# Optimization experiments

Hardware: AMD Instinct MI355X
Metric: run time of the kernel (lower is better)

The kernel has to match this reference:

```python
import jax, jax.numpy as jnp
import numpy as np

RADIUS = 1.3
RES = 256
N_INT = 128
STEP = 0.02


def grid_sample3d(grid, coords):
    # grid: [C, D, H, W]; coords: [N, 3] as (x, y, z) in [-1, 1]
    # trilinear, align_corners=True, border clamp (torch grid_sample semantics)
    D, H, W = grid.shape[1], grid.shape[2], grid.shape[3]

    def to_idx(c, size):
        return jnp.clip((c + 1.0) * 0.5 * (size - 1), 0.0, size - 1.0)

    x = to_idx(coords[:, 0], W)
    y = to_idx(coords[:, 1], H)
    z = to_idx(coords[:, 2], D)
    x0 = jnp.floor(x).astype(jnp.int32)
    y0 = jnp.floor(y).astype(jnp.int32)
    z0 = jnp.floor(z).astype(jnp.int32)
    x1 = jnp.minimum(x0 + 1, W - 1)
    y1 = jnp.minimum(y0 + 1, H - 1)
    z1 = jnp.minimum(z0 + 1, D - 1)
    wx = x - x0.astype(x.dtype)
    wy = y - y0.astype(y.dtype)
    wz = z - z0.astype(z.dtype)

    def g(zi, yi, xi):
        return grid[:, zi, yi, xi]  # [C, N]

    c00 = g(z0, y0, x0) * (1 - wx) + g(z0, y0, x1) * wx
    c01 = g(z0, y1, x0) * (1 - wx) + g(z0, y1, x1) * wx
    c10 = g(z1, y0, x0) * (1 - wx) + g(z1, y0, x1) * wx
    c11 = g(z1, y1, x0) * (1 - wx) + g(z1, y1, x1) * wx
    c0 = c00 * (1 - wy) + c01 * wy
    c1 = c10 * (1 - wy) + c11 * wy
    return (c0 * (1 - wz) + c1 * wz).T  # [N, C]


def sh16(d):
    # real spherical harmonics, degree 4 (instant-ngp / tcnn convention), d unit
    x, y, z = d[:, 0], d[:, 1], d[:, 2]
    xx, yy, zz = x * x, y * y, z * z
    xy, yz, xz = x * y, y * z, x * z
    return jnp.stack([
        jnp.full_like(x, 0.28209479177387814),
        -0.48860251190291987 * y,
        0.48860251190291987 * z,
        -0.48860251190291987 * x,
        1.0925484305920792 * xy,
        -1.0925484305920792 * yz,
        0.94617469575755997 * zz - 0.31539156525251999,
        -1.0925484305920792 * xz,
        0.54627421529603959 * (xx - yy),
        0.59004358992664352 * y * (-3.0 * xx + yy),
        2.8906114426405538 * xy * z,
        0.45704579946446572 * y * (1.0 - 5.0 * zz),
        0.3731763325901154 * z * (5.0 * zz - 3.0),
        0.45704579946446572 * x * (1.0 - 5.0 * zz),
        1.445305721320277 * z * (xx - yy),
        0.59004358992664352 * x * (-xx + 3.0 * yy),
    ], axis=-1)  # [N, 16]


def mlp3(x, W0, W1, W2):
    # FullyFusedMLP: no bias, ReLU hidden, linear output
    h = jnp.maximum(x @ W0, 0.0)
    h = jnp.maximum(h @ W1, 0.0)
    return h @ W2


def setup_inputs() -> dict:
    key = jax.random.key(0)
    k = jax.random.split(key, 10)
    B, FD, NF = 4096, 32, 16
    rays_o = jax.random.normal(k[0], (B, 3), jnp.float32) * 0.5
    rays_d = jax.random.normal(k[1], (B, 3), jnp.float32)
    G1 = jax.random.normal(k[2], (3, RES, RES, RES), jnp.float32) * 0.02
    F = jax.random.normal(k[3], (FD, NF, NF, NF), jnp.float32) * 0.05
    W_sig0 = jax.random.normal(k[4], (FD, 128), jnp.float32) / np.sqrt(FD).astype(np.float32)
    W_sig1 = jax.random.normal(k[5], (128, 128), jnp.float32) / np.float32(np.sqrt(128))
    W_sig2 = jax.random.normal(k[6], (128, 16), jnp.float32) / np.float32(np.sqrt(128))
    W_col0 = jax.random.normal(k[7], (31, 64), jnp.float32) / np.float32(np.sqrt(31))
    W_col1 = jax.random.normal(k[8], (64, 64), jnp.float32) / np.float32(np.sqrt(64))
    W_col2 = jax.random.normal(k[9], (64, 3), jnp.float32) / np.float32(np.sqrt(64))
    return {"rays_o": rays_o, "rays_d": rays_d, "G1": G1, "F": F,
            "W_sig0": W_sig0, "W_sig1": W_sig1, "W_sig2": W_sig2,
            "W_col0": W_col0, "W_col1": W_col1, "W_col2": W_col2}


def reference(rays_o, rays_d, G1, F, W_sig0, W_sig1, W_sig2, W_col0, W_col1, W_col2):
    B = rays_o.shape[0]
    d = rays_d / jnp.linalg.norm(rays_d, axis=-1, keepdims=True)
    # ray-sphere intersection |o + t d| = RADIUS (unit d)
    b = jnp.sum(rays_o * d, axis=-1)
    c = jnp.sum(rays_o * rays_o, axis=-1) - RADIUS ** 2
    disc = b * b - c
    hit = disc > 0
    s = jnp.sqrt(jnp.where(hit, disc, 1.0))
    tmin = jnp.where(hit, jnp.maximum(-b - s, 0.0), 0.0)
    tmax = jnp.where(hit, -b + s, 0.0)
    t = tmin[:, None] + jnp.arange(N_INT + 1, dtype=jnp.float32)[None, :] * STEP  # [B, n+1]
    tmid = 0.5 * (t[:, :-1] + t[:, 1:])  # [B, n]
    mask = hit[:, None] & (tmid <= tmax[:, None])  # [B, n]
    pts = rays_o[:, None, :] + d[:, None, :] * tmid[..., None]  # [B, n, 3]
    coords = (pts / RADIUS).reshape(-1, 3)  # in [-1, 1]
    # hash/indirection lookup: G1 gives learned coords into feature grid F
    g1 = grid_sample3d(G1, coords)        # [N, 3]
    feats = grid_sample3d(F, g1)          # [N, 32]
    sig_out = mlp3(feats, W_sig0, W_sig1, W_sig2)  # [N, 16]
    sigma = jnp.where(mask, sig_out[:, 0].reshape(B, N_INT), 0.0)
    sigma = jnp.maximum(sigma, 0.0)
    pd = jnp.broadcast_to(d[:, None, :], (B, N_INT, 3)).reshape(-1, 3)
    enc = sh16(pd)
    col_raw = mlp3(jnp.concatenate([enc, sig_out[:, 1:]], axis=-1), W_col0, W_col1, W_col2)
    col = jnp.where(mask[..., None], col_raw.reshape(B, N_INT, 3), 0.0)
    # volume rendering (sigma2alpha + shrgb2rgb with white background)
    alpha = 1.0 - jnp.exp(-sigma * STEP)
    T = jnp.cumprod(1.0 - alpha + 1e-10, axis=1)
    T_excl = jnp.concatenate([jnp.ones((B, 1), alpha.dtype), T[:, :-1]], axis=1)
    w = alpha * T_excl
    rgb = jnp.einsum('bn,bnc->bc', w, jax.nn.sigmoid(col))
    rgb = rgb + (1.0 - jnp.sum(w, axis=1, keepdims=True))
    return rgb
```

## Files before the change

### kernel.cpp

```cpp
#include <hip/hip_runtime.h>
#include <stdint.h>

#define STEP 0.02f
#define INV_RADIUS (1.0f/1.3f)
#define RADIUS 1.3f

typedef __bf16   bf16x8 __attribute__((ext_vector_type(8)));
typedef float    f32x4  __attribute__((ext_vector_type(4)));
typedef uint32_t u32x4  __attribute__((ext_vector_type(4)));

#define FT_OFF   0
#define W0_OFF   262144
#define W1_OFF   270336
#define W2_OFF   303104
#define C0_OFF   307200
#define C1_OFF   311296
#define C2_OFF   319488

#define FE_OFF    0
#define SIG_OFF   4096
#define COL_OFF   4608
#define WAVE_LDS  6656

__device__ __forceinline__ uint32_t pack2(float a, float b){
    uint32_t ua = __float_as_uint(a); ua += 0x7FFFu + ((ua>>16)&1u);
    uint32_t ub = __float_as_uint(b); ub += 0x7FFFu + ((ub>>16)&1u);
    return (ua>>16) | (ub & 0xFFFF0000u);
}
__device__ __forceinline__ void toidx(float c, float sizem1, int isize,
                                      int& i0, int& i1, float& w){
    float t = (c + 1.f) * 0.5f * sizem1;
    t = fminf(fmaxf(t, 0.f), sizem1);
    float f = floorf(t);
    i0 = (int)f;
    i1 = i0 + 1; if (i1 > isize - 1) i1 = isize - 1;
    w = t - f;
}
__device__ __forceinline__ void lds_fence(){
    asm volatile("s_waitcnt lgkmcnt(0)" ::: "memory");
}
__device__ __forceinline__ uint32_t cvtpk(float lo, float hi){
    uint32_t r;
    asm("v_cvt_pk_bf16_f32 %0, %1, %2" : "=v"(r) : "v"(lo), "v"(hi));
    return r;
}
__device__ __forceinline__ void p32swap(uint32_t& a, uint32_t& b){
    asm("v_permlane32_swap_b32 %0, %1" : "+v"(a), "+v"(b));
}
__device__ __forceinline__ void p16swap(uint32_t& a, uint32_t& b){
    asm("v_permlane16_swap_b32 %0, %1" : "+v"(a), "+v"(b));
}
__device__ __forceinline__ uint32_t pkrelu(float a, float b){
    return cvtpk(fmaxf(a, 0.f), fmaxf(b, 0.f));
}
__device__ __forceinline__ bf16x8 frag_from(uint32_t a, uint32_t b, uint32_t c, uint32_t d){
    union { u32x4 u; bf16x8 h; } cv;
    cv.u = (u32x4){a, b, c, d};
    return cv.h;
}
__device__ __forceinline__ bf16x8 xpose4(const f32x4& t0, const f32x4& t1){
    uint32_t A = pkrelu(t0[0], t0[1]);
    uint32_t B = pkrelu(t0[2], t0[3]);
    uint32_t C = pkrelu(t1[0], t1[1]);
    uint32_t D = pkrelu(t1[2], t1[3]);
    p32swap(A, C); p16swap(A, C);
    p32swap(B, D); p16swap(B, D);
    return frag_from(A, B, C, D);
}

__global__ __launch_bounds__(256) void prep_f(const float* __restrict__ F, uint32_t* __restrict__ ws){
    int idx = blockIdx.x * 256 + threadIdx.x;
    if (idx >= 4096) return;
    uint32_t o[16];
    #pragma unroll
    for (int c = 0; c < 16; c++){
        float a = F[(2*c  )*4096 + idx];
        float b = F[(2*c+1)*4096 + idx];
        o[c] = pack2(a, b);
    }
    uint4* dst = (uint4*)ws;
    #pragma unroll
    for (int q = 0; q < 4; q++)
        dst[idx*4 + q] = make_uint4(o[q*4], o[q*4+1], o[q*4+2], o[q*4+3]);
}

__global__ __launch_bounds__(256) void prep_w(const float* __restrict__ W0, const float* __restrict__ W1,
                                              const float* __restrict__ W2, const float* __restrict__ Wc0,
                                              const float* __restrict__ Wc1, const float* __restrict__ Wc2,
                                              char* __restrict__ ws){
    int gid = blockIdx.x * 256 + threadIdx.x;
    if (gid >= 58*64) return;
    int cg = gid >> 6, lane = gid & 63;
    const float* src; int K, N, base_cg, dstoff;
    if      (cg < 8)  { src = W0;  K = 32;  N = 128; base_cg = 0;  dstoff = W0_OFF; }
    else if (cg < 40) { src = W1;  K = 128; N = 128; base_cg = 8;  dstoff = W1_OFF; }
    else if (cg < 44) { src = W2;  K = 128; N = 16;  base_cg = 40; dstoff = W2_OFF; }
    else if (cg < 48) { src = Wc0; K = 31;  N = 64;  base_cg = 44; dstoff = C0_OFF; }
    else if (cg < 56) { src = Wc1; K = 64;  N = 64;  base_cg = 48; dstoff = C1_OFF; }
    else              { src = Wc2; K = 64;  N = 3;   base_cg = 56; dstoff = C2_OFF; }
    bool c0remap = (cg >= 44 && cg < 48);
    int local = cg - base_cg;
    int NT = (N + 15) >> 4;
    int nt = local % NT, kk = local / NT;
    int n = nt*16 + (lane & 15);
    int kbase = kk*32 + (lane >> 4)*8;
    uint32_t o[4];
    #pragma unroll
    for (int jj = 0; jj < 4; jj++){
        int k0 = kbase + jj*2, k1 = k0 + 1;
        int k0s = (c0remap && k0 > 16) ? k0 - 1 : k0;
        int k1s = (c0remap && k1 > 16) ? k1 - 1 : k1;
        bool v0 = (n < N) && (k0s < K) && !(c0remap && k0 == 16);
        bool v1 = (n < N) && (k1s < K) && !(c0remap && k1 == 16);
        float a = v0 ? src[k0s*N + n] : 0.f;
        float b = v1 ? src[k1s*N + n] : 0.f;
        o[jj] = pack2(a, b);
    }
    uint4* dst = (uint4*)(ws + dstoff);
    dst[local*64 + lane] = make_uint4(o[0], o[1], o[2], o[3]);
}

__global__ __launch_bounds__(128, 3)
void nerf_fused(const float* __restrict__ rays_o, const float* __restrict__ rays_d,
                const float* __restrict__ G1, const char* __restrict__ ws,
                float* __restrict__ out){
    __shared__ __align__(16) char smem[WAVE_LDS*2];
    const int tid  = threadIdx.x;
    const int wv   = tid >> 6;
    const int lane = tid & 63;
    const int nl   = lane & 15;
    const int quad = lane >> 4;
    const int ray  = blockIdx.x*2 + wv;
    char* WB = smem + wv*WAVE_LDS;

    float ox = rays_o[ray*3+0], oy = rays_o[ray*3+1], oz = rays_o[ray*3+2];
    float rx = rays_d[ray*3+0], ry = rays_d[ray*3+1], rz = rays_d[ray*3+2];
    float nrm = sqrtf(rx*rx + ry*ry + rz*rz);
    float dx = rx/nrm, dy = ry/nrm, dz = rz/nrm;
    float bq = ox*dx + oy*dy + oz*dz;
    float cq = ox*ox + oy*oy + oz*oz - RADIUS*RADIUS;
    float disc = bq*bq - cq;
    bool  hit = disc > 0.f;
    float sq   = sqrtf(hit ? disc : 1.f);
    float tmin = hit ? fmaxf(-bq - sq, 0.f) : 0.f;
    float tmax = hit ? (-bq + sq) : 0.f;

    uint32_t encw0, encw1, encw2, encw3, cinmask;
    {
        float xx=dx*dx, yy=dy*dy, zz=dz*dz, xy=dx*dy, yz=dy*dz, xz=dx*dz;
        float sh0 = 0.28209479177387814f;
        float sh1 = -0.48860251190291987f*dy;
        float sh2 =  0.48860251190291987f*dz;
        float sh3 = -0.48860251190291987f*dx;
        float sh4 =  1.0925484305920792f*xy;
        float sh5 = -1.0925484305920792f*yz;
        float sh6 =  0.94617469575756f*zz - 0.31539156525252f;
        float sh7 = -1.0925484305920792f*xz;
        float sh8 =  0.5462742152960396f*(xx-yy);
        float sh9 =  0.5900435899266435f*dy*(-3.f*xx+yy);
        float sh10 = 2.890611442640554f*xy*dz;
        float sh11 = 0.4570457994644657f*dy*(1.f-5.f*zz);
        float sh12 = 0.3731763325901154f*dz*(5.f*zz-3.f);
        float sh13 = 0.4570457994644657f*dx*(1.f-5.f*zz);
        float sh14 = 1.445305721320277f*dz*(xx-yy);
        float sh15 = 0.5900435899266435f*dx*(-xx+3.f*yy);
        bool q0 = (quad == 0);
        encw0 = q0 ? pack2(sh0, sh1) : pack2(sh8,  sh9);
        encw1 = q0 ? pack2(sh2, sh3) : pack2(sh10, sh11);
        encw2 = q0 ? pack2(sh4, sh5) : pack2(sh12, sh13);
        encw3 = q0 ? pack2(sh6, sh7) : pack2(sh14, sh15);
        cinmask = (quad == 2) ? 0xFFFF0000u : 0xFFFFFFFFu;
    }

    const char* pW0 = ws + W0_OFF; const char* pW1 = ws + W1_OFF; const char* pW2 = ws + W2_OFF;
    const char* pC0 = ws + C0_OFF; const char* pC1 = ws + C1_OFF; const char* pC2 = ws + C2_OFF;
    const f32x4 vzero = {0.f, 0.f, 0.f, 0.f};
    float* SIGf = (float*)(WB + SIG_OFF);
    float* COLf = (float*)(WB + COL_OFF);

    #define RD_A(bp, linRow, m) \
        (*(const bf16x8*)((bp) + (linRow)*64 + ((quad ^ (((m)>>1)&3))*16)))
    #define LD_B(base, kk, NT, nt) \
        (*(const bf16x8*)((base) + (((kk)*(NT) + (nt))*64 + lane)*16))

    float Dn = (tmax - tmin) * (1.0f/STEP);
    int nv = (int)fminf(128.f, fmaxf(0.f, floorf(Dn + 0.5f) + 1.f));
    int nhalf = (nv > 64) ? 2 : 1;

    for (int half = 0; half < nhalf; half++){
        lds_fence();
        {
            int p = half*64 + lane;
            if (p < nv){
                float tmid = tmin + ((float)p + 0.5f) * STEP;
                float px = (ox + dx*tmid) * INV_RADIUS;
                float py = (oy + dy*tmid) * INV_RADIUS;
                float pz = (oz + dz*tmid) * INV_RADIUS;
                int x0,x1,y0,y1,z0,z1; float wx,wy,wz;
                toidx(px, 255.f, 256, x0, x1, wx);
                toidx(py, 255.f, 256, y0, y1, wy);
                toidx(pz, 255.f, 256, z0, z1, wz);
                float g1v[3];
                #pragma unroll
                for (int ch = 0; ch < 3; ch++){
                    const float* gp = G1 + ch*16777216;
                    int b00 = (z0*256 + y0)*256, b01 = (z0*256 + y1)*256;
                    int b10 = (z1*256 + y0)*256, b11 = (z1*256 + y1)*256;
                    float c000 = gp[b00+x0], c001 = gp[b00+x1];
                    float c010 = gp[b01+x0], c011 = gp[b01+x1];
                    float c100 = gp[b10+x0], c101 = gp[b10+x1];
                    float c110 = gp[b11+x0], c111 = gp[b11+x1];
                    float c00 = c000 + (c001-c000)*wx;
                    float c01 = c010 + (c011-c010)*wx;
                    float c10 = c100 + (c101-c100)*wx;
                    float c11 = c110 + (c111-c110)*wx;
                    float c0 = c00 + (c01-c00)*wy;
                    float c1 = c10 + (c11-c10)*wy;
                    g1v[ch] = c0 + (c1-c0)*wz;
                }
                int fx0,fx1,fy0,fy1,fz0,fz1; float fwx,fwy,fwz;
                toidx(g1v[0], 15.f, 16, fx0, fx1, fwx);
                toidx(g1v[1], 15.f, 16, fy0, fy1, fwy);
                toidx(g1v[2], 15.f, 16, fz0, fz1, fwz);
                float feats[32];
                #pragma unroll
                for (int i = 0; i < 32; i++) feats[i] = 0.f;
                const uint4* Ft = (const uint4*)(ws + FT_OFF);
                #pragma unroll 2
                for (int corner = 0; corner < 8; corner++){
                    int cz = (corner>>2)&1, cy = (corner>>1)&1, cx = corner&1;
                    int xi = cx?fx1:fx0, yi = cy?fy1:fy0, zi = cz?fz1:fz0;
                    float w = (cx?fwx:1.f-fwx) * (cy?fwy:1.f-fwy) * (cz?fwz:1.f-fwz);
                    const uint4* cp = Ft + ((zi*16 + yi)*16 + xi)*4;
                    #pragma unroll
                    for (int q = 0; q < 4; q++){
                        uint4 v = cp[q];
                        uint32_t u[4] = {v.x, v.y, v.z, v.w};
                        #pragma unroll
                        for (int e = 0; e < 4; e++){
                            feats[q*8 + e*2    ] += w * __uint_as_float(u[e] << 16);
                            feats[q*8 + e*2 + 1] += w * __uint_as_float(u[e] & 0xFFFF0000u);
                        }
                    }
                }
                int fsw = (lane>>1)&3;
                #pragma unroll
                for (int c = 0; c < 4; c++){
                    uint4 v = make_uint4(pack2(feats[c*8+0], feats[c*8+1]),
                                         pack2(feats[c*8+2], feats[c*8+3]),
                                         pack2(feats[c*8+4], feats[c*8+5]),
                                         pack2(feats[c*8+6], feats[c*8+7]));
                    *(uint4*)(WB + FE_OFF + lane*64 + ((c^fsw)*16)) = v;
                }
            }
        }
        lds_fence();

        bf16x8 bW2[4], bC0[4], bC2[2];
        #pragma unroll
        for (int kk = 0; kk < 4; kk++) bW2[kk] = LD_B(pW2, kk, 1, 0);
        #pragma unroll
        for (int nt = 0; nt < 4; nt++) bC0[nt] = LD_B(pC0, 0, 4, nt);
        #pragma unroll
        for (int kk = 0; kk < 2; kk++) bC2[kk] = LD_B(pC2, kk, 1, 0);

        int rem = nv - half*64;
        int mtmax = (rem >= 64) ? 4 : ((rem + 15) >> 4);
        #pragma unroll 1
        for (int mt = 0; mt < mtmax; mt++){
            const int mArow = mt*16 + nl;
            const int tb = half*64 + mt*16;

            bf16x8 fe = RD_A(WB + FE_OFF, mArow, mArow);
            f32x4 a0[8];
            #pragma unroll
            for (int nt = 0; nt < 8; nt++)
                a0[nt] = __builtin_amdgcn_mfma_f32_16x16x32_bf16(LD_B(pW0,0,8,nt), fe, vzero, 0,0,0);
            bf16x8 h1[4];
            #pragma unroll
            for (int kk = 0; kk < 4; kk++)
                h1[kk] = xpose4(a0[2*kk], a0[2*kk+1]);

            f32x4 a1[8];
            #pragma unroll
            for (int nt = 0; nt < 8; nt++) a1[nt] = vzero;
            #pragma unroll
            for (int kk = 0; kk < 4; kk++)
                #pragma unroll
                for (int nt = 0; nt < 8; nt++)
                    a1[nt] = __builtin_amdgcn_mfma_f32_16x16x32_bf16(LD_B(pW1,kk,8,nt), h1[kk], a1[nt], 0,0,0);
            bf16x8 h2[4];
            #pragma unroll
            for (int kk = 0; kk < 4; kk++)
                h2[kk] = xpose4(a1[2*kk], a1[2*kk+1]);

            f32x4 sacc = vzero;
            #pragma unroll
            for (int kk = 0; kk < 4; kk++)
                sacc = __builtin_amdgcn_mfma_f32_16x16x32_bf16(bW2[kk], h2[kk], sacc, 0,0,0);
            if (quad == 0) SIGf[tb + nl] = sacc[0];

            uint32_t ca = cvtpk(sacc[0], sacc[1]);
            uint32_t cb = cvtpk(sacc[2], sacc[3]);
            p32swap(ca, cb); p16swap(ca, cb);
            uint32_t cw0 = encw0, cw2 = encw2;
            p32swap(cw0, ca);
            p32swap(cw2, cb);
            cw0 &= cinmask;
            uint32_t cw1 = (quad < 2) ? encw1 : ca;
            uint32_t cw3 = (quad < 2) ? encw3 : cb;
            bf16x8 cin = frag_from(cw0, cw1, cw2, cw3);

            f32x4 c0[4];
            #pragma unroll
            for (int nt = 0; nt < 4; nt++)
                c0[nt] = __builtin_amdgcn_mfma_f32_16x16x32_bf16(bC0[nt], cin, vzero, 0,0,0);
            bf16x8 g1[2];
            #pragma unroll
            for (int kk = 0; kk < 2; kk++)
                g1[kk] = xpose4(c0[2*kk], c0[2*kk+1]);

            f32x4 c1[4];
            #pragma unroll
            for (int nt = 0; nt < 4; nt++) c1[nt] = vzero;
            #pragma unroll
            for (int kk = 0; kk < 2; kk++)
                #pragma unroll
                for (int nt = 0; nt < 4; nt++)
                    c1[nt] = __builtin_amdgcn_mfma_f32_16x16x32_bf16(LD_B(pC1,kk,4,nt), g1[kk], c1[nt], 0,0,0);
            bf16x8 g2[2];
            #pragma unroll
            for (int kk = 0; kk < 2; kk++)
                g2[kk] = xpose4(c1[2*kk], c1[2*kk+1]);

            f32x4 cc = vzero;
            #pragma unroll
            for (int kk = 0; kk < 2; kk++)
                cc = __builtin_amdgcn_mfma_f32_16x16x32_bf16(bC2[kk], g2[kk], cc, 0,0,0);
            if (quad == 0){
                *(float2*)(COLf + (tb + nl)*4) = make_float2(cc[0], cc[1]);
                COLf[(tb + nl)*4 + 2] = cc[2];
            }
        }
    }
    lds_fence();

    float t0 = tmin + ((float)lane + 0.5f) * STEP;
    float t1 = tmin + ((float)(lane + 64) + 0.5f) * STEP;
    bool  m0 = hit && (t0 <= tmax);
    bool  m1 = hit && (t1 <= tmax);
    float sig0 = m0 ? fmaxf(SIGf[lane], 0.f) : 0.f;
    float sig1 = m1 ? fmaxf(SIGf[lane + 64], 0.f) : 0.f;
    float e0 = expf(-sig0 * STEP), e1 = expf(-sig1 * STEP);
    float al0 = 1.f - e0, al1 = 1.f - e1;
    float li0 = logf(e0 + 1e-10f), li1 = logf(e1 + 1e-10f);
    float incl0 = li0, incl1 = li1;
    #pragma unroll
    for (int off = 1; off < 64; off <<= 1){
        float v0 = __shfl_up(incl0, off);
        float v1 = __shfl_up(incl1, off);
        if (lane >= off){ incl0 += v0; incl1 += v1; }
    }
    float tot0 = __shfl(incl0, 63);
    float ex0 = incl0 - li0;
    float ex1 = tot0 + incl1 - li1;
    float w0 = al0 * expf(ex0);
    float w1 = al1 * expf(ex1);
    float cr0 = m0 ? COLf[lane*4+0] : 0.f;
    float cg0 = m0 ? COLf[lane*4+1] : 0.f;
    float cb0 = m0 ? COLf[lane*4+2] : 0.f;
    float cr1 = m1 ? COLf[(lane+64)*4+0] : 0.f;
    float cg1 = m1 ? COLf[(lane+64)*4+1] : 0.f;
    float cb1 = m1 ? COLf[(lane+64)*4+2] : 0.f;
    float r = w0 / (1.f + expf(-cr0)) + w1 / (1.f + expf(-cr1));
    float g = w0 / (1.f + expf(-cg0)) + w1 / (1.f + expf(-cg1));
    float b = w0 / (1.f + expf(-cb0)) + w1 / (1.f + expf(-cb1));
    float wa = w0 + w1;
    #pragma unroll
    for (int off = 32; off > 0; off >>= 1){
        r  += __shfl_xor(r,  off);
        g  += __shfl_xor(g,  off);
        b  += __shfl_xor(b,  off);
        wa += __shfl_xor(wa, off);
    }
    if (lane == 0){
        out[ray*3+0] = r + (1.f - wa);
        out[ray*3+1] = g + (1.f - wa);
        out[ray*3+2] = b + (1.f - wa);
    }
    #undef RD_A
    #undef LD_B
}

extern "C" void kernel_launch(void* const* d_in, const int* in_sizes, int n_in,
                              void* d_out, int out_size, void* d_ws, size_t ws_size,
                              hipStream_t stream){
    const float* rays_o = (const float*)d_in[0];
    const float* rays_d = (const float*)d_in[1];
    const float* G1     = (const float*)d_in[2];
    const float* F      = (const float*)d_in[3];
    prep_f<<<16, 256, 0, stream>>>(F, (uint32_t*)d_ws);
    prep_w<<<15, 256, 0, stream>>>((const float*)d_in[4], (const float*)d_in[5],
                                   (const float*)d_in[6], (const float*)d_in[7],
                                   (const float*)d_in[8], (const float*)d_in[9],
                                   (char*)d_ws);
    nerf_fused<<<2048, 128, 0, stream>>>(rays_o, rays_d, G1, (const char*)d_ws, (float*)d_out);
}
```

Baseline: 428.6 us.

## Split each ray's samples across two waves in a block instead of one ray per wave

Each block now processes one ray, with wave 0 handling samples 0-63 and wave 1 handling samples 64-127. Sigma and color results go to shared LDS buffers, and after a block barrier only wave 0 does the compositing scan. The grid doubles to 4096 blocks and the occupancy hint rises from 3 to 4. This is meant to cut the serial latency of the per-ray two-half loop and expose more parallelism, but wave 1 sits idle during compositing and does no work at all for short rays.

```diff
diff --git a/kernel.cpp b/kernel.cpp
--- a/kernel.cpp
+++ b/kernel.cpp
@@ -17,10 +17,10 @@
 #define C1_OFF   311296
 #define C2_OFF   319488
 
-#define FE_OFF    0
-#define SIG_OFF   4096
-#define COL_OFF   4608
-#define WAVE_LDS  6656
+#define FE_BYTES  4096
+#define SIG_OFF   8192
+#define COL_OFF   8704
+#define BLOCK_LDS 10752
 
 __device__ __forceinline__ uint32_t pack2(float a, float b){
     uint32_t ua = __float_as_uint(a); ua += 0x7FFFu + ((ua>>16)&1u);
@@ -120,18 +120,20 @@
     dst[local*64 + lane] = make_uint4(o[0], o[1], o[2], o[3]);
 }
 
-__global__ __launch_bounds__(128, 3)
+__global__ __launch_bounds__(128, 4)
 void nerf_fused(const float* __restrict__ rays_o, const float* __restrict__ rays_d,
                 const float* __restrict__ G1, const char* __restrict__ ws,
                 float* __restrict__ out){
-    __shared__ __align__(16) char smem[WAVE_LDS*2];
+    __shared__ __align__(16) char smem[BLOCK_LDS];
     const int tid  = threadIdx.x;
     const int wv   = tid >> 6;
     const int lane = tid & 63;
     const int nl   = lane & 15;
     const int quad = lane >> 4;
-    const int ray  = blockIdx.x*2 + wv;
-    char* WB = smem + wv*WAVE_LDS;
+    const int ray  = blockIdx.x;
+    char*  FEB  = smem + wv*FE_BYTES;
+    float* SIGf = (float*)(smem + SIG_OFF);
+    float* COLf = (float*)(smem + COL_OFF);
 
     float ox = rays_o[ray*3+0], oy = rays_o[ray*3+1], oz = rays_o[ray*3+2];
     float rx = rays_d[ray*3+0], ry = rays_d[ray*3+1], rz = rays_d[ray*3+2];
@@ -175,8 +177,6 @@
     const char* pW0 = ws + W0_OFF; const char* pW1 = ws + W1_OFF; const char* pW2 = ws + W2_OFF;
     const char* pC0 = ws + C0_OFF; const char* pC1 = ws + C1_OFF; const char* pC2 = ws + C2_OFF;
     const f32x4 vzero = {0.f, 0.f, 0.f, 0.f};
-    float* SIGf = (float*)(WB + SIG_OFF);
-    float* COLf = (float*)(WB + COL_OFF);
 
     #define RD_A(bp, linRow, m) \
         (*(const bf16x8*)((bp) + (linRow)*64 + ((quad ^ (((m)>>1)&3))*16)))
@@ -185,13 +185,13 @@
 
     float Dn = (tmax - tmin) * (1.0f/STEP);
     int nv = (int)fminf(128.f, fmaxf(0.f, floorf(Dn + 0.5f) + 1.f));
-    int nhalf = (nv > 64) ? 2 : 1;
-
-    for (int half = 0; half < nhalf; half++){
-        lds_fence();
+    int rem = nv - wv*64;
+    if (rem > 64) rem = 64;
+
+    if (rem > 0){
         {
-            int p = half*64 + lane;
-            if (p < nv){
+            if (lane < rem){
+                int p = wv*64 + lane;
                 float tmid = tmin + ((float)p + 0.5f) * STEP;
                 float px = (ox + dx*tmid) * INV_RADIUS;
                 float py = (oy + dy*tmid) * INV_RADIUS;
@@ -250,7 +250,7 @@
                                          pack2(feats[c*8+2], feats[c*8+3]),
                                          pack2(feats[c*8+4], feats[c*8+5]),
                                          pack2(feats[c*8+6], feats[c*8+7]));
-                    *(uint4*)(WB + FE_OFF + lane*64 + ((c^fsw)*16)) = v;
+                    *(uint4*)(FEB + lane*64 + ((c^fsw)*16)) = v;
                 }
             }
         }
@@ -264,14 +264,13 @@
         #pragma unroll
         for (int kk = 0; kk < 2; kk++) bC2[kk] = LD_B(pC2, kk, 1, 0);
 
-        int rem = nv - half*64;
-        int mtmax = (rem >= 64) ? 4 : ((rem + 15) >> 4);
+        int mtmax = (rem + 15) >> 4;
         #pragma unroll 1
         for (int mt = 0; mt < mtmax; mt++){
             const int mArow = mt*16 + nl;
-            const int tb = half*64 + mt*16;
-
-            bf16x8 fe = RD_A(WB + FE_OFF, mArow, mArow);
+            const int tb = wv*64 + mt*16;
+
+            bf16x8 fe = RD_A(FEB, mArow, mArow);
             f32x4 a0[8];
             #pragma unroll
             for (int nt = 0; nt < 8; nt++)
@@ -343,7 +342,10 @@
             }
         }
     }
-    lds_fence();
+
+    __syncthreads();
+
+    if (wv != 0) return;
 
     float t0 = tmin + ((float)lane + 0.5f) * STEP;
     float t1 = tmin + ((float)(lane + 64) + 0.5f) * STEP;
@@ -404,5 +406,5 @@
                                    (const float*)d_in[6], (const float*)d_in[7],
                                    (const float*)d_in[8], (const float*)d_in[9],
                                    (char*)d_ws);
-    nerf_fused<<<2048, 128, 0, stream>>>(rays_o, rays_d, G1, (const char*)d_ws, (float*)d_out);
-}
+    nerf_fused<<<4096, 128, 0, stream>>>(rays_o, rays_d, G1, (const char*)d_ws, (float*)d_out);
+}
```

Result: no change. 428.5 us (-0.0%).
